# Kernel optimization log

Measured on AMD Instinct MI355X. Metric: run time of the kernel, lower is better.

Reference implementation:

```python
import jax, jax.numpy as jnp
import numpy as np

HID, NH, NKV, HD, BASE = 1536, 24, 6, 64, 10000.0
G = NH // NKV  # kv groups


def setup_inputs() -> dict:
    key = jax.random.key(0)
    k1, k2, k3, k4, k5 = jax.random.split(key, 5)
    B, S = 2, 2048
    s = 0.02
    return {
        "hidden_states": jax.random.normal(k1, (B, S, HID), jnp.float32),
        "position_ids": jnp.broadcast_to(jnp.arange(S, dtype=jnp.int64)[None, :], (B, S)),
        "Wq": jax.random.normal(k2, (NH * HD, HID), jnp.float32) * s,
        "Wk": jax.random.normal(k3, (NKV * HD, HID), jnp.float32) * s,
        "Wv": jax.random.normal(k4, (NKV * HD, HID), jnp.float32) * s,
        "Wo": jax.random.normal(k5, (HID, NH * HD), jnp.float32) * s,
    }


def _rope_tables(seq_len, dtype):
    inv_freq = 1.0 / (BASE ** (jnp.arange(0, HD, 2, dtype=jnp.float32) / HD))
    t = jnp.arange(seq_len, dtype=jnp.float32)
    freqs = jnp.einsum("i,j->ij", t, inv_freq)          # [S, HD/2]
    emb = jnp.concatenate([freqs, freqs], axis=-1)       # [S, HD]
    return jnp.cos(emb).astype(dtype), jnp.sin(emb).astype(dtype)


def _rotate_half(x):
    x1, x2 = x[..., : HD // 2], x[..., HD // 2:]
    return jnp.concatenate([-x2, x1], axis=-1)


def reference(hidden_states, position_ids, Wq, Wk, Wv, Wo):
    B, S, _ = hidden_states.shape
    q = (hidden_states @ Wq.T).reshape(B, S, NH, HD).transpose(0, 2, 1, 3)   # [B,NH,S,D]
    k = (hidden_states @ Wk.T).reshape(B, S, NKV, HD).transpose(0, 2, 1, 3)  # [B,NKV,S,D]
    v = (hidden_states @ Wv.T).reshape(B, S, NKV, HD).transpose(0, 2, 1, 3)

    cos_t, sin_t = _rope_tables(S, hidden_states.dtype)
    cos = cos_t[position_ids][:, None]  # [B,1,S,D]
    sin = sin_t[position_ids][:, None]
    q = q * cos + _rotate_half(q) * sin
    k = k * cos + _rotate_half(k) * sin

    # GQA attention without materializing repeated K/V: view q as [B,NKV,G,S,D]
    qg = q.reshape(B, NKV, G, S, HD)
    scale = 1.0 / np.sqrt(HD)
    scores = jnp.einsum("bkgsd,bktd->bkgst", qg, k) * scale  # [B,NKV,G,S,S]
    causal = jnp.tril(jnp.ones((S, S), dtype=bool))
    scores = jnp.where(causal, scores, jnp.finfo(scores.dtype).min)
    probs = jax.nn.softmax(scores, axis=-1)
    out = jnp.einsum("bkgst,bktd->bkgsd", probs, v)          # [B,NKV,G,S,D]
    out = out.reshape(B, NH, S, HD).transpose(0, 2, 1, 3).reshape(B, S, NH * HD)
    return out @ Wo.T
```

## Files before the change

kernel.cpp:

```cpp
#include <hip/hip_runtime.h>
#include <hip/hip_bf16.h>

#define HIDN 1536
#define NH   24
#define NKV  6
#define HD   64
#define BB   2
#define SS   2048
#define MTOT (BB*SS)
#define NQKV 2304
#define NCHUNK 80
#define LOG2E 1.4426950408889634f

typedef __bf16 bf16x8 __attribute__((ext_vector_type(8)));
typedef float  f32x4  __attribute__((ext_vector_type(4)));
typedef unsigned short u16x8 __attribute__((ext_vector_type(8)));
typedef unsigned int   u32x2 __attribute__((ext_vector_type(2)));

typedef __attribute__((address_space(1))) const unsigned short as1_ushort;
typedef __attribute__((address_space(3))) unsigned short as3_ushort;

__device__ inline float bf2f(unsigned short u) {
    unsigned v = (unsigned)u << 16; float f; __builtin_memcpy(&f, &v, 4); return f;
}
__device__ inline unsigned short f2bf(float f) {
    unsigned u; __builtin_memcpy(&u, &f, 4);
    u = (u + 0x7FFFu + ((u >> 16) & 1u)) >> 16;
    return (unsigned short)u;
}
__device__ inline unsigned cvt_pk_bf16(float lo, float hi) {
    unsigned r;
    asm("v_cvt_pk_bf16_f32 %0, %1, %2" : "=v"(r) : "v"(lo), "v"(hi));
    return r;
}
__device__ inline float exp2_hw(float x) {
    float r;
    asm("v_exp_f32 %0, %1" : "=v"(r) : "v"(x));
    return r;
}
__device__ inline float rowmax16_dpp(float x) {
    int v, r;
    v = __float_as_int(x);
    r = __builtin_amdgcn_update_dpp(v, v, 0x121, 0xF, 0xF, false);
    x = fmaxf(x, __int_as_float(r));
    v = __float_as_int(x);
    r = __builtin_amdgcn_update_dpp(v, v, 0x122, 0xF, 0xF, false);
    x = fmaxf(x, __int_as_float(r));
    v = __float_as_int(x);
    r = __builtin_amdgcn_update_dpp(v, v, 0x124, 0xF, 0xF, false);
    x = fmaxf(x, __int_as_float(r));
    v = __float_as_int(x);
    r = __builtin_amdgcn_update_dpp(v, v, 0x128, 0xF, 0xF, false);
    x = fmaxf(x, __int_as_float(r));
    return x;
}

__global__ __launch_bounds__(256) void k_prep(const float* __restrict__ h_f,
                                              const float* __restrict__ Wq,
                                              const float* __restrict__ Wk,
                                              const float* __restrict__ Wv,
                                              const float* __restrict__ Wo,
                                              unsigned short* __restrict__ h_bf,
                                              unsigned short* __restrict__ qkv_w,
                                              unsigned short* __restrict__ Wo_bf,
                                              float2* __restrict__ cs) {
    int i = blockIdx.x * 256 + threadIdx.x;
    const int nH = MTOT * HIDN / 4;
    const int nQ = HIDN * HIDN / 4;
    const int nK = NKV * HD * HIDN / 4;
    const int nW = 2 * nQ + 2 * nK;
    if (i < nH + nW) {
        const float* src; unsigned short* dst; int j;
        if (i < nH)                    { src = h_f; dst = h_bf;                        j = i; }
        else if ((i -= nH) < nQ)       { src = Wq;  dst = qkv_w;                       j = i; }
        else if (i < nQ + nK)          { src = Wk;  dst = qkv_w + (size_t)nQ * 4;      j = i - nQ; }
        else if (i < nQ + 2 * nK)      { src = Wv;  dst = qkv_w + (size_t)(nQ + nK) * 4; j = i - nQ - nK; }
        else                           { src = Wo;  dst = Wo_bf;                       j = i - nQ - 2 * nK; }
        float4 v = reinterpret_cast<const float4*>(src)[j];
        ushort4 o;
        o.x = f2bf(v.x); o.y = f2bf(v.y); o.z = f2bf(v.z); o.w = f2bf(v.w);
        reinterpret_cast<ushort4*>(dst)[j] = o;
        return;
    }
    int k = i - (nH + nW);
    if (k < SS * 32) {
        int s = k >> 5, f = k & 31;
        double inv = pow(10000.0, -(double)f / 32.0);
        double ang = (double)s * inv;
        cs[k] = make_float2((float)cos(ang), (float)sin(ang));
    }
}

template <typename OutT>
__global__ __launch_bounds__(256) void gemm_bt(const unsigned short* __restrict__ A,
                                               const unsigned short* __restrict__ Bt,
                                               OutT* __restrict__ C,
                                               int N, int K) {
    __shared__ unsigned short Alds[128 * 64];
    __shared__ unsigned short Blds[128 * 64];
    int t = threadIdx.x;
    int lane = t & 63, w = t >> 6;
    int m0 = blockIdx.y * 128, n0 = blockIdx.x * 128;
    int wm = (w >> 1) * 64, wn = (w & 1) * 64;
    int cidx = lane & 15, quad = lane >> 4;
    int srow = lane >> 3, scol = (lane & 7) * 8;

    f32x4 zero = {0.f, 0.f, 0.f, 0.f};
    f32x4 acc[4][4];
#pragma unroll
    for (int mi = 0; mi < 4; ++mi)
#pragma unroll
        for (int ni = 0; ni < 4; ++ni) acc[mi][ni] = zero;

    for (int k0 = 0; k0 < K; k0 += 64) {
        __syncthreads();
#pragma unroll
        for (int c = 0; c < 4; ++c) {
            int chunk = w + c * 4;
            int row = chunk * 8 + srow;
            int col = scol ^ ((row & 7) * 8);
            __builtin_amdgcn_global_load_lds(
                (as1_ushort*)(A + (size_t)(m0 + row) * K + k0 + col),
                (as3_ushort*)&Alds[chunk * 512], 16, 0, 0);
            __builtin_amdgcn_global_load_lds(
                (as1_ushort*)(Bt + (size_t)(n0 + row) * K + k0 + col),
                (as3_ushort*)&Blds[chunk * 512], 16, 0, 0);
        }
        __syncthreads();
#pragma unroll
        for (int ka = 0; ka < 2; ++ka) {
            bf16x8 af[4], bfr[4];
#pragma unroll
            for (int mi = 0; mi < 4; ++mi) {
                int arow = wm + mi * 16 + cidx;
                af[mi] = *reinterpret_cast<bf16x8*>(
                    &Alds[arow * 64 + ((ka * 32 + quad * 8) ^ ((arow & 7) * 8))]);
            }
#pragma unroll
            for (int ni = 0; ni < 4; ++ni) {
                int brow = wn + ni * 16 + cidx;
                bfr[ni] = *reinterpret_cast<bf16x8*>(
                    &Blds[brow * 64 + ((ka * 32 + quad * 8) ^ ((brow & 7) * 8))]);
            }
#pragma unroll
            for (int mi = 0; mi < 4; ++mi)
#pragma unroll
                for (int ni = 0; ni < 4; ++ni)
                    acc[mi][ni] = __builtin_amdgcn_mfma_f32_16x16x32_bf16(af[mi], bfr[ni],
                                                                          acc[mi][ni], 0, 0, 0);
        }
    }
#pragma unroll
    for (int mi = 0; mi < 4; ++mi)
#pragma unroll
        for (int ni = 0; ni < 4; ++ni)
#pragma unroll
            for (int i = 0; i < 4; ++i) {
                int row = m0 + wm + mi * 16 + quad * 4 + i;
                int col = n0 + wn + ni * 16 + cidx;
                C[(size_t)row * N + col] = acc[mi][ni][i];
            }
}

__global__ __launch_bounds__(256) void gemm_qkv(const unsigned short* __restrict__ A,
                                                const unsigned short* __restrict__ Bt,
                                                const int* __restrict__ pos_ids,
                                                const float2* __restrict__ cs,
                                                unsigned short* __restrict__ q_p,
                                                unsigned short* __restrict__ k_p,
                                                unsigned short* __restrict__ v_p) {
    __shared__ unsigned short Alds[128 * 64];
    __shared__ unsigned short Blds[128 * 64];
    int t = threadIdx.x;
    int lane = t & 63, w = t >> 6;
    int m0 = blockIdx.y * 128, n0 = blockIdx.x * 128;
    int wm = (w >> 1) * 64, wn = (w & 1) * 64;
    int cidx = lane & 15, quad = lane >> 4;
    int srow = lane >> 3, scol = (lane & 7) * 8;

    f32x4 zero = {0.f, 0.f, 0.f, 0.f};
    f32x4 acc[4][4];
#pragma unroll
    for (int mi = 0; mi < 4; ++mi)
#pragma unroll
        for (int ni = 0; ni < 4; ++ni) acc[mi][ni] = zero;

    for (int k0 = 0; k0 < HIDN; k0 += 64) {
        __syncthreads();
#pragma unroll
        for (int c = 0; c < 4; ++c) {
            int chunk = w + c * 4;
            int row = chunk * 8 + srow;
            int col = scol ^ ((row & 7) * 8);
            __builtin_amdgcn_global_load_lds(
                (as1_ushort*)(A + (size_t)(m0 + row) * HIDN + k0 + col),
                (as3_ushort*)&Alds[chunk * 512], 16, 0, 0);
            __builtin_amdgcn_global_load_lds(
                (as1_ushort*)(Bt + (size_t)(n0 + row) * HIDN + k0 + col),
                (as3_ushort*)&Blds[chunk * 512], 16, 0, 0);
        }
        __syncthreads();
#pragma unroll
        for (int ka = 0; ka < 2; ++ka) {
            bf16x8 af[4], bfr[4];
#pragma unroll
            for (int mi = 0; mi < 4; ++mi) {
                int arow = wm + mi * 16 + cidx;
                af[mi] = *reinterpret_cast<bf16x8*>(
                    &Alds[arow * 64 + ((ka * 32 + quad * 8) ^ ((arow & 7) * 8))]);
            }
#pragma unroll
            for (int ni = 0; ni < 4; ++ni) {
                int brow = wn + ni * 16 + cidx;
                bfr[ni] = *reinterpret_cast<bf16x8*>(
                    &Blds[brow * 64 + ((ka * 32 + quad * 8) ^ ((brow & 7) * 8))]);
            }
#pragma unroll
            for (int mi = 0; mi < 4; ++mi)
#pragma unroll
                for (int ni = 0; ni < 4; ++ni)
                    acc[mi][ni] = __builtin_amdgcn_mfma_f32_16x16x32_bf16(af[mi], bfr[ni],
                                                                          acc[mi][ni], 0, 0, 0);
        }
    }

    int colbase = n0 + wn;
    if (colbase >= NH * HD + NKV * HD) {
        int h = (colbase - (NH * HD + NKV * HD)) >> 6;
#pragma unroll
        for (int mi = 0; mi < 4; ++mi)
#pragma unroll
            for (int i = 0; i < 4; ++i) {
                int row = m0 + wm + mi * 16 + quad * 4 + i;
                int b = row >> 11, s = row & 2047;
                size_t base = ((size_t)(b * NKV + h) * SS + s) * 64;
#pragma unroll
                for (int ni = 0; ni < 4; ++ni)
                    v_p[base + ni * 16 + cidx] = f2bf(acc[mi][ni][i]);
            }
    } else {
        bool isQ = colbase < NH * HD;
        unsigned short* dst = isQ ? q_p : k_p;
        int h = isQ ? (colbase >> 6) : ((colbase - NH * HD) >> 6);
        int H = isQ ? NH : NKV;
        float scl = isQ ? (0.125f * LOG2E) : 1.0f;
#pragma unroll
        for (int mi = 0; mi < 4; ++mi)
#pragma unroll
            for (int i = 0; i < 4; ++i) {
                int row = m0 + wm + mi * 16 + quad * 4 + i;
                int b = row >> 11, s = row & 2047;
                int pos = pos_ids[row];
                float2 c1 = cs[pos * 32 + cidx];
                float2 c2 = cs[pos * 32 + 16 + cidx];
                size_t base = ((size_t)(b * H + h) * SS + s) * 64;
                float x10 = acc[mi][0][i], x20 = acc[mi][2][i];
                float x11 = acc[mi][1][i], x21 = acc[mi][3][i];
                dst[base + cidx]       = f2bf((x10 * c1.x - x20 * c1.y) * scl);
                dst[base + 32 + cidx]  = f2bf((x20 * c1.x + x10 * c1.y) * scl);
                dst[base + 16 + cidx]  = f2bf((x11 * c2.x - x21 * c2.y) * scl);
                dst[base + 48 + cidx]  = f2bf((x21 * c2.x + x11 * c2.y) * scl);
            }
    }
}

#define TRR(dst, ADDR, OFF) asm volatile("ds_read_b64_tr_b16 %0, %1 offset:" #OFF \
                                         : "=v"(dst) : "v"(ADDR))

__global__ __launch_bounds__(256, 4) void k_attn(const unsigned short* __restrict__ Qp,
                                                 const unsigned short* __restrict__ Kp,
                                                 const unsigned short* __restrict__ Vp,
                                                 unsigned short* __restrict__ part_acc,
                                                 float* __restrict__ part_ml,
                                                 unsigned short* __restrict__ a_out) {
    int bxr = NCHUNK - 1 - (int)blockIdx.x;
    int h = blockIdx.y, b = blockIdx.z;
    int kvh = h >> 2;
    int qt = 0, c = 0, g;
    {
        g = (bxr >= 48) ? 3 : (bxr >= 24) ? 2 : (bxr >= 8) ? 1 : 0;
        int b0 = 4 * g * (g + 1);
        int idx = bxr - b0;
        qt = 8 * g + idx / (g + 1);
        c = idx % (g + 1);
    }
    int p = (b * NH + h) * NCHUNK + bxr;
    int qbase = qt * 64, ck0 = c * 512;
    int nt = min(8, qt + 1 - c * 8);

    int t = threadIdx.x, lane = t & 63, w = t >> 6;
    int cidx = lane & 15, quad = lane >> 4;
    int qrow0 = qbase + w * 16;

    const unsigned short* qptr  = Qp + ((size_t)(b * NH + h) * SS + qrow0) * HD;
    const unsigned short* kbase = Kp + (((size_t)(b * NKV + kvh) * SS) + ck0) * HD;
    const unsigned short* vbase = Vp + (((size_t)(b * NKV + kvh) * SS) + ck0) * HD;

    __shared__ unsigned short Klds[2 * 4096];
    __shared__ unsigned short Vt[2 * 4096];
    __shared__ unsigned short Pt[4][64 * 16];

    const unsigned short* ksrc[2];
    const unsigned short* vsrc[2];
#pragma unroll
    for (int i = 0; i < 2; ++i) {
        int o = (w * 2 + i) * 512 + lane * 8;
        int kh = o >> 10, ka_ = (o >> 9) & 1, kq = (o >> 7) & 3, kc = (o >> 3) & 15;
        ksrc[i] = kbase + (kh * 16 + kc) * HD + ka_ * 32 + kq * 8;
        int r = o & 1023;
        int kv = ((r >> 6) << 2) | ((r >> 4) & 3);
        int d  = ((o >> 10) << 4) | (r & 15);
        vsrc[i] = vbase + kv * HD + d;
    }

    bf16x8 qa[2];
#pragma unroll
    for (int ka = 0; ka < 2; ++ka)
        qa[ka] = *reinterpret_cast<const bf16x8*>(qptr + (size_t)cidx * HD + ka * 32 + quad * 8);

    bf16x8 ones;
    {
        unsigned short ob = 0x3F80;
        u16x8 ov;
#pragma unroll
        for (int j = 0; j < 8; ++j) ov[j] = ob;
        __builtin_memcpy(&ones, &ov, 16);
    }

    f32x4 zero = {0.f, 0.f, 0.f, 0.f};
    f32x4 acc[4], acc_l = zero;
    float m_run[4];
#pragma unroll
    for (int i = 0; i < 4; ++i) { acc[i] = zero; m_run[i] = -1e30f; }

#pragma unroll
    for (int i = 0; i < 2; ++i) {
        __builtin_amdgcn_global_load_lds((as1_ushort*)ksrc[i],
                                         (as3_ushort*)&Klds[(w * 2 + i) * 512], 16, 0, 0);
        __builtin_amdgcn_global_load_lds((as1_ushort*)vsrc[i],
                                         (as3_ushort*)&Vt[(w * 2 + i) * 512], 16, 0, 0);
    }
    asm volatile("s_waitcnt vmcnt(0)" ::: "memory");
    __syncthreads();

    unsigned vtb  = (unsigned)(uintptr_t)(as3_ushort*)&Vt[0];
    unsigned va_base = vtb + (unsigned)(quad * 256 + cidx * 8);
    unsigned ptb  = (unsigned)(uintptr_t)(as3_ushort*)&Pt[w][0];
    unsigned va_p = ptb + (unsigned)(quad * 256 + cidx * 8);
    char* pwr = (char*)&Pt[w][0] + cidx * 32 + quad * 8;

    for (int it = 0; it < nt; ++it) {
        int cur = it & 1;
        int kvb = ck0 + it * 64;

        if (it + 1 < nt) {
            size_t nv = (size_t)(it + 1) * 64 * HD;
#pragma unroll
            for (int i = 0; i < 2; ++i) {
                __builtin_amdgcn_global_load_lds(
                    (as1_ushort*)(ksrc[i] + nv),
                    (as3_ushort*)&Klds[(cur ^ 1) * 4096 + (w * 2 + i) * 512], 16, 0, 0);
                __builtin_amdgcn_global_load_lds(
                    (as1_ushort*)(vsrc[i] + nv),
                    (as3_ushort*)&Vt[(cur ^ 1) * 4096 + (w * 2 + i) * 512], 16, 0, 0);
            }
        }

        bf16x8 kb[4][2];
#pragma unroll
        for (int ht = 0; ht < 4; ++ht)
#pragma unroll
            for (int ka = 0; ka < 2; ++ka)
                kb[ht][ka] = *reinterpret_cast<bf16x8*>(
                    &Klds[cur * 4096 + ht * 1024 + ka * 512 + quad * 128 + cidx * 8]);
        f32x4 sc[4];
#pragma unroll
        for (int ht = 0; ht < 4; ++ht) {
            f32x4 cacc = zero;
            cacc = __builtin_amdgcn_mfma_f32_16x16x32_bf16(qa[0], kb[ht][0], cacc, 0, 0, 0);
            cacc = __builtin_amdgcn_mfma_f32_16x16x32_bf16(qa[1], kb[ht][1], cacc, 0, 0, 0);
            sc[ht] = cacc;
        }

        unsigned va = va_base + (unsigned)(cur * 8192);
        u32x2 tv[4][4];
        TRR(tv[0][0], va, 0);    TRR(tv[0][1], va, 128);
        TRR(tv[0][2], va, 1024); TRR(tv[0][3], va, 1152);
        TRR(tv[1][0], va, 2048); TRR(tv[1][1], va, 2176);
        TRR(tv[1][2], va, 3072); TRR(tv[1][3], va, 3200);
        TRR(tv[2][0], va, 4096); TRR(tv[2][1], va, 4224);
        TRR(tv[2][2], va, 5120); TRR(tv[2][3], va, 5248);
        TRR(tv[3][0], va, 6144); TRR(tv[3][1], va, 6272);
        TRR(tv[3][2], va, 7168); TRR(tv[3][3], va, 7296);

        if (kvb + 63 > qrow0) {
#pragma unroll
            for (int ht = 0; ht < 4; ++ht)
#pragma unroll
                for (int i = 0; i < 4; ++i)
                    if (kvb + ht * 16 + cidx > qrow0 + quad * 4 + i) sc[ht][i] = -1e30f;
        }

        float mx[4];
#pragma unroll
        for (int i = 0; i < 4; ++i) {
            mx[i] = fmaxf(fmaxf(sc[0][i], sc[1][i]), fmaxf(sc[2][i], sc[3][i]));
            mx[i] = rowmax16_dpp(mx[i]);
        }

        bool need = false;
#pragma unroll
        for (int i = 0; i < 4; ++i) need |= (mx[i] > m_run[i] + 11.5f);
        if (__any(need)) {
#pragma unroll
            for (int i = 0; i < 4; ++i) {
                float mnew = fmaxf(m_run[i], mx[i]);
                float scl = exp2_hw(m_run[i] - mnew);
                m_run[i] = mnew;
#pragma unroll
                for (int dt = 0; dt < 4; ++dt) acc[dt][i] *= scl;
                acc_l[i] *= scl;
            }
        }
#pragma unroll
        for (int i = 0; i < 4; ++i)
#pragma unroll
            for (int ht = 0; ht < 4; ++ht) sc[ht][i] = exp2_hw(sc[ht][i] - m_run[i]);

#pragma unroll
        for (int ht = 0; ht < 4; ++ht) {
            u32x2 pk;
            pk[0] = cvt_pk_bf16(sc[ht][0], sc[ht][1]);
            pk[1] = cvt_pk_bf16(sc[ht][2], sc[ht][3]);
            *reinterpret_cast<u32x2*>(pwr + ht * 512) = pk;
        }
        asm volatile("" ::: "memory");
        u32x2 pt_[4];
        TRR(pt_[0], va_p, 0);    TRR(pt_[1], va_p, 128);
        TRR(pt_[2], va_p, 1024); TRR(pt_[3], va_p, 1152);
        asm volatile("s_waitcnt lgkmcnt(0)" ::: "memory");
        __builtin_amdgcn_sched_barrier(0);

        union { u32x2 a[2]; bf16x8 v; } up0, up1;
        up0.a[0] = pt_[0]; up0.a[1] = pt_[1];
        up1.a[0] = pt_[2]; up1.a[1] = pt_[3];
        bf16x8 pa0 = up0.v, pa1 = up1.v;

        __builtin_amdgcn_s_setprio(1);
        acc_l = __builtin_amdgcn_mfma_f32_16x16x32_bf16(pa0, ones, acc_l, 0, 0, 0);
        acc_l = __builtin_amdgcn_mfma_f32_16x16x32_bf16(pa1, ones, acc_l, 0, 0, 0);
#pragma unroll
        for (int dt = 0; dt < 4; ++dt) {
            union { u32x2 a[2]; bf16x8 v; } u0, u1;
            u0.a[0] = tv[dt][0]; u0.a[1] = tv[dt][1];
            u1.a[0] = tv[dt][2]; u1.a[1] = tv[dt][3];
            acc[dt] = __builtin_amdgcn_mfma_f32_16x16x32_bf16(pa0, u0.v, acc[dt], 0, 0, 0);
            acc[dt] = __builtin_amdgcn_mfma_f32_16x16x32_bf16(pa1, u1.v, acc[dt], 0, 0, 0);
        }
        __builtin_amdgcn_s_setprio(0);

        asm volatile("s_waitcnt vmcnt(0)" ::: "memory");
        __syncthreads();
    }

    if (g == 0) {
        float rl[4];
#pragma unroll
        for (int i = 0; i < 4; ++i) rl[i] = 1.f / acc_l[i];
#pragma unroll
        for (int dt = 0; dt < 4; ++dt)
#pragma unroll
            for (int i = 0; i < 4; ++i) {
                int row = qrow0 + quad * 4 + i;
                size_t o = ((size_t)(b * SS) + row) * HIDN + h * HD + dt * 16 + cidx;
                a_out[o] = f2bf(acc[dt][i] * rl[i]);
            }
    } else {
#pragma unroll
        for (int dt = 0; dt < 4; ++dt)
#pragma unroll
            for (int i = 0; i < 4; ++i) {
                int row = w * 16 + quad * 4 + i;
                part_acc[((size_t)p * 64 + row) * 64 + dt * 16 + cidx] = f2bf(acc[dt][i]);
            }
        if (cidx == 0) {
#pragma unroll
            for (int i = 0; i < 4; ++i) {
                int row = w * 16 + quad * 4 + i;
                part_ml[((size_t)p * 64 + row) * 2 + 0] = m_run[i];
                part_ml[((size_t)p * 64 + row) * 2 + 1] = acc_l[i];
            }
        }
    }
}

__global__ __launch_bounds__(256) void k_combine(const unsigned short* __restrict__ part_acc,
                                                 const float* __restrict__ part_ml,
                                                 unsigned short* __restrict__ a_out) {
    int idx = blockIdx.x * 256 + threadIdx.x;
    int d = idx & 63;
    int tmp = idx >> 6;
    int h = tmp % NH;
    int m2 = tmp / NH;
    int b = m2 / (SS - 512);
    int s = 512 + m2 % (SS - 512);
    int qt = s >> 6, row = s & 63;
    int g = qt >> 3;
    int off = 4 * g * (g + 1) + (qt & 7) * (g + 1);
    int C = g + 1;
    int pb = (b * NH + h) * NCHUNK + off;

    float2 ml[4];
    float M = -1e30f;
#pragma unroll
    for (int cc = 0; cc < 4; ++cc) {
        if (cc < C) {
            ml[cc] = *reinterpret_cast<const float2*>(&part_ml[((size_t)(pb + cc) * 64 + row) * 2]);
            M = fmaxf(M, ml[cc].x);
        } else {
            ml[cc] = make_float2(-1e30f, 0.f);
        }
    }
    float L = 0.f, O = 0.f;
#pragma unroll
    for (int cc = 0; cc < 4; ++cc) {
        if (cc < C) {
            float wgt = exp2_hw(ml[cc].x - M);
            L += ml[cc].y * wgt;
            O += bf2f(part_acc[((size_t)(pb + cc) * 64 + row) * 64 + d]) * wgt;
        }
    }
    a_out[((size_t)(b * SS) + s) * HIDN + h * 64 + d] = f2bf(O / L);
}

extern "C" void kernel_launch(void* const* d_in, const int* in_sizes, int n_in,
                              void* d_out, int out_size, void* d_ws, size_t ws_size,
                              hipStream_t stream) {
    (void)in_sizes; (void)n_in; (void)out_size; (void)ws_size;
    const float* h_f  = (const float*)d_in[0];
    const int*   pos  = (const int*)d_in[1];
    const float* Wq_f = (const float*)d_in[2];
    const float* Wk_f = (const float*)d_in[3];
    const float* Wv_f = (const float*)d_in[4];
    const float* Wo_f = (const float*)d_in[5];
    float* out = (float*)d_out;

    char* ws = (char*)d_ws;
    size_t off = 0;
    auto alloc = [&](size_t bytes) -> void* {
        void* p = ws + off;
        off += (bytes + 255) & ~(size_t)255;
        return p;
    };
    unsigned short* region0 = (unsigned short*)alloc((size_t)48 * NCHUNK * 64 * 64 * 2);
    unsigned short* h_bf     = region0;
    unsigned short* part_acc = region0;
    unsigned short* qkv_w  = (unsigned short*)alloc((size_t)NQKV * HIDN * 2);
    unsigned short* Wo_bf  = (unsigned short*)alloc((size_t)HIDN * NH * HD * 2);
    unsigned short* q_p    = (unsigned short*)alloc((size_t)MTOT * NH * HD * 2);
    unsigned short* k_p    = (unsigned short*)alloc((size_t)MTOT * NKV * HD * 2);
    unsigned short* v_p    = (unsigned short*)alloc((size_t)MTOT * NKV * HD * 2);
    unsigned short* a_out  = (unsigned short*)alloc((size_t)MTOT * HIDN * 2);
    float2* cs = (float2*)alloc((size_t)SS * 32 * 8);
    float* part_ml = (float*)alloc((size_t)BB * NH * NCHUNK * 64 * 2 * 4);

    {
        int nH = MTOT * HIDN / 4;
        int nW = 2 * (HIDN * HIDN / 4) + 2 * (NKV * HD * HIDN / 4);
        int total = nH + nW + SS * 32;
        k_prep<<<total / 256, 256, 0, stream>>>(h_f, Wq_f, Wk_f, Wv_f, Wo_f,
                                                h_bf, qkv_w, Wo_bf, cs);
    }

    gemm_qkv<<<dim3(NQKV / 128, MTOT / 128), 256, 0, stream>>>(
        h_bf, qkv_w, pos, cs, q_p, k_p, v_p);

    k_attn<<<dim3(NCHUNK, NH, BB), 256, 0, stream>>>(q_p, k_p, v_p, part_acc, part_ml, a_out);
    k_combine<<<(MTOT * NH * HD * 3 / 4) / 256, 256, 0, stream>>>(part_acc, part_ml, a_out);

    gemm_bt<float><<<dim3(HIDN / 128, MTOT / 128), 256, 0, stream>>>(
        a_out, Wo_bf, out, HIDN, HIDN);
}
```

Baseline: 209.2 us.

## Double-buffer LDS tiles in GEMM kernels to overlap loads with MFMA

Both the generic GEMM and the fused QKV GEMM now use two LDS buffers per operand, prefetching the next K tile with global_load_lds while MFMAs run on the current one. The per-tile load offsets are precomputed once, and the pre-load barrier is replaced by a vmcnt wait plus a single barrier at the end of each iteration. This is meant to hide global memory latency behind compute. It doubles LDS use to 64KB per block, which may reduce occupancy.

```diff
diff --git a/kernel.cpp b/kernel.cpp
--- a/kernel.cpp
+++ b/kernel.cpp
@@ -96,8 +96,8 @@
                                                const unsigned short* __restrict__ Bt,
                                                OutT* __restrict__ C,
                                                int N, int K) {
-    __shared__ unsigned short Alds[128 * 64];
-    __shared__ unsigned short Blds[128 * 64];
+    __shared__ unsigned short Alds[2][128 * 64];
+    __shared__ unsigned short Blds[2][128 * 64];
     int t = threadIdx.x;
     int lane = t & 63, w = t >> 6;
     int m0 = blockIdx.y * 128, n0 = blockIdx.x * 128;
@@ -105,6 +105,16 @@
     int cidx = lane & 15, quad = lane >> 4;
     int srow = lane >> 3, scol = (lane & 7) * 8;
 
+    int srcoff[4], dstoff[4];
+#pragma unroll
+    for (int c = 0; c < 4; ++c) {
+        int chunk = w + c * 4;
+        int row = chunk * 8 + srow;
+        int col = scol ^ ((row & 7) * 8);
+        srcoff[c] = row * K + col;
+        dstoff[c] = chunk * 512;
+    }
+
     f32x4 zero = {0.f, 0.f, 0.f, 0.f};
     f32x4 acc[4][4];
 #pragma unroll
@@ -112,21 +122,32 @@
 #pragma unroll
         for (int ni = 0; ni < 4; ++ni) acc[mi][ni] = zero;
 
-    for (int k0 = 0; k0 < K; k0 += 64) {
-        __syncthreads();
-#pragma unroll
-        for (int c = 0; c < 4; ++c) {
-            int chunk = w + c * 4;
-            int row = chunk * 8 + srow;
-            int col = scol ^ ((row & 7) * 8);
-            __builtin_amdgcn_global_load_lds(
-                (as1_ushort*)(A + (size_t)(m0 + row) * K + k0 + col),
-                (as3_ushort*)&Alds[chunk * 512], 16, 0, 0);
-            __builtin_amdgcn_global_load_lds(
-                (as1_ushort*)(Bt + (size_t)(n0 + row) * K + k0 + col),
-                (as3_ushort*)&Blds[chunk * 512], 16, 0, 0);
-        }
-        __syncthreads();
+    const unsigned short* Ab = A + (size_t)m0 * K;
+    const unsigned short* Bb = Bt + (size_t)n0 * K;
+
+#pragma unroll
+    for (int c = 0; c < 4; ++c) {
+        __builtin_amdgcn_global_load_lds((as1_ushort*)(Ab + srcoff[c]),
+                                         (as3_ushort*)&Alds[0][dstoff[c]], 16, 0, 0);
+        __builtin_amdgcn_global_load_lds((as1_ushort*)(Bb + srcoff[c]),
+                                         (as3_ushort*)&Blds[0][dstoff[c]], 16, 0, 0);
+    }
+    asm volatile("s_waitcnt vmcnt(0)" ::: "memory");
+    __syncthreads();
+
+    int nk = K >> 6;
+    for (int kt = 0; kt < nk; ++kt) {
+        int cur = kt & 1;
+        if (kt + 1 < nk) {
+            int koff = (kt + 1) * 64;
+#pragma unroll
+            for (int c = 0; c < 4; ++c) {
+                __builtin_amdgcn_global_load_lds((as1_ushort*)(Ab + srcoff[c] + koff),
+                                                 (as3_ushort*)&Alds[cur ^ 1][dstoff[c]], 16, 0, 0);
+                __builtin_amdgcn_global_load_lds((as1_ushort*)(Bb + srcoff[c] + koff),
+                                                 (as3_ushort*)&Blds[cur ^ 1][dstoff[c]], 16, 0, 0);
+            }
+        }
 #pragma unroll
         for (int ka = 0; ka < 2; ++ka) {
             bf16x8 af[4], bfr[4];
@@ -134,13 +155,13 @@
             for (int mi = 0; mi < 4; ++mi) {
                 int arow = wm + mi * 16 + cidx;
                 af[mi] = *reinterpret_cast<bf16x8*>(
-                    &Alds[arow * 64 + ((ka * 32 + quad * 8) ^ ((arow & 7) * 8))]);
+                    &Alds[cur][arow * 64 + ((ka * 32 + quad * 8) ^ ((arow & 7) * 8))]);
             }
 #pragma unroll
             for (int ni = 0; ni < 4; ++ni) {
                 int brow = wn + ni * 16 + cidx;
                 bfr[ni] = *reinterpret_cast<bf16x8*>(
-                    &Blds[brow * 64 + ((ka * 32 + quad * 8) ^ ((brow & 7) * 8))]);
+                    &Blds[cur][brow * 64 + ((ka * 32 + quad * 8) ^ ((brow & 7) * 8))]);
             }
 #pragma unroll
             for (int mi = 0; mi < 4; ++mi)
@@ -149,6 +170,8 @@
                     acc[mi][ni] = __builtin_amdgcn_mfma_f32_16x16x32_bf16(af[mi], bfr[ni],
                                                                           acc[mi][ni], 0, 0, 0);
         }
+        asm volatile("s_waitcnt vmcnt(0)" ::: "memory");
+        __syncthreads();
     }
 #pragma unroll
     for (int mi = 0; mi < 4; ++mi)
@@ -169,8 +192,8 @@
                                                 unsigned short* __restrict__ q_p,
                                                 unsigned short* __restrict__ k_p,
                                                 unsigned short* __restrict__ v_p) {
-    __shared__ unsigned short Alds[128 * 64];
-    __shared__ unsigned short Blds[128 * 64];
+    __shared__ unsigned short Alds[2][128 * 64];
+    __shared__ unsigned short Blds[2][128 * 64];
     int t = threadIdx.x;
     int lane = t & 63, w = t >> 6;
     int m0 = blockIdx.y * 128, n0 = blockIdx.x * 128;
@@ -178,6 +201,16 @@
     int cidx = lane & 15, quad = lane >> 4;
     int srow = lane >> 3, scol = (lane & 7) * 8;
 
+    int srcoff[4], dstoff[4];
+#pragma unroll
+    for (int c = 0; c < 4; ++c) {
+        int chunk = w + c * 4;
+        int row = chunk * 8 + srow;
+        int col = scol ^ ((row & 7) * 8);
+        srcoff[c] = row * HIDN + col;
+        dstoff[c] = chunk * 512;
+    }
+
     f32x4 zero = {0.f, 0.f, 0.f, 0.f};
     f32x4 acc[4][4];
 #pragma unroll
@@ -185,21 +218,32 @@
 #pragma unroll
         for (int ni = 0; ni < 4; ++ni) acc[mi][ni] = zero;
 
-    for (int k0 = 0; k0 < HIDN; k0 += 64) {
-        __syncthreads();
-#pragma unroll
-        for (int c = 0; c < 4; ++c) {
-            int chunk = w + c * 4;
-            int row = chunk * 8 + srow;
-            int col = scol ^ ((row & 7) * 8);
-            __builtin_amdgcn_global_load_lds(
-                (as1_ushort*)(A + (size_t)(m0 + row) * HIDN + k0 + col),
-                (as3_ushort*)&Alds[chunk * 512], 16, 0, 0);
-            __builtin_amdgcn_global_load_lds(
-                (as1_ushort*)(Bt + (size_t)(n0 + row) * HIDN + k0 + col),
-                (as3_ushort*)&Blds[chunk * 512], 16, 0, 0);
-        }
-        __syncthreads();
+    const unsigned short* Ab = A + (size_t)m0 * HIDN;
+    const unsigned short* Bb = Bt + (size_t)n0 * HIDN;
+
+#pragma unroll
+    for (int c = 0; c < 4; ++c) {
+        __builtin_amdgcn_global_load_lds((as1_ushort*)(Ab + srcoff[c]),
+                                         (as3_ushort*)&Alds[0][dstoff[c]], 16, 0, 0);
+        __builtin_amdgcn_global_load_lds((as1_ushort*)(Bb + srcoff[c]),
+                                         (as3_ushort*)&Blds[0][dstoff[c]], 16, 0, 0);
+    }
+    asm volatile("s_waitcnt vmcnt(0)" ::: "memory");
+    __syncthreads();
+
+    const int nk = HIDN >> 6;
+    for (int kt = 0; kt < nk; ++kt) {
+        int cur = kt & 1;
+        if (kt + 1 < nk) {
+            int koff = (kt + 1) * 64;
+#pragma unroll
+            for (int c = 0; c < 4; ++c) {
+                __builtin_amdgcn_global_load_lds((as1_ushort*)(Ab + srcoff[c] + koff),
+                                                 (as3_ushort*)&Alds[cur ^ 1][dstoff[c]], 16, 0, 0);
+                __builtin_amdgcn_global_load_lds((as1_ushort*)(Bb + srcoff[c] + koff),
+                                                 (as3_ushort*)&Blds[cur ^ 1][dstoff[c]], 16, 0, 0);
+            }
+        }
 #pragma unroll
         for (int ka = 0; ka < 2; ++ka) {
             bf16x8 af[4], bfr[4];
@@ -207,13 +251,13 @@
             for (int mi = 0; mi < 4; ++mi) {
                 int arow = wm + mi * 16 + cidx;
                 af[mi] = *reinterpret_cast<bf16x8*>(
-                    &Alds[arow * 64 + ((ka * 32 + quad * 8) ^ ((arow & 7) * 8))]);
+                    &Alds[cur][arow * 64 + ((ka * 32 + quad * 8) ^ ((arow & 7) * 8))]);
             }
 #pragma unroll
             for (int ni = 0; ni < 4; ++ni) {
                 int brow = wn + ni * 16 + cidx;
                 bfr[ni] = *reinterpret_cast<bf16x8*>(
-                    &Blds[brow * 64 + ((ka * 32 + quad * 8) ^ ((brow & 7) * 8))]);
+                    &Blds[cur][brow * 64 + ((ka * 32 + quad * 8) ^ ((brow & 7) * 8))]);
             }
 #pragma unroll
             for (int mi = 0; mi < 4; ++mi)
@@ -222,6 +266,8 @@
                     acc[mi][ni] = __builtin_amdgcn_mfma_f32_16x16x32_bf16(af[mi], bfr[ni],
                                                                           acc[mi][ni], 0, 0, 0);
         }
+        asm volatile("s_waitcnt vmcnt(0)" ::: "memory");
+        __syncthreads();
     }
 
     int colbase = n0 + wn;
```

Measured after the change: 205.0 us. 1.02x faster.
